# Kernel tuning notes

Hardware: AMD Instinct MI355X
Metric: run time of the kernel (lower is better)

The kernel has to match this reference:

```python
import jax, jax.numpy as jnp
import numpy as np

B, L, H = 2, 2048, 1024
NH, KVH = 16, 4
HD = H // NH          # 64
G = NH // KVH         # 4 query heads per kv head


def setup_inputs() -> dict:
    key = jax.random.key(0)
    ks = jax.random.split(key, 10)
    s = 0.02
    return {
        "hidden_states": jax.random.normal(ks[0], (B, L, H), dtype=jnp.float32),
        "attention_mask": jnp.zeros((B, 1, L, L), dtype=jnp.float32),
        "Wq": jax.random.normal(ks[1], (H, H), dtype=jnp.float32) * s,
        "bq": jnp.zeros((H,), dtype=jnp.float32),
        "Wk": jax.random.normal(ks[2], (KVH * HD, H), dtype=jnp.float32) * s,
        "bk": jnp.zeros((KVH * HD,), dtype=jnp.float32),
        "Wv": jax.random.normal(ks[3], (KVH * HD, H), dtype=jnp.float32) * s,
        "bv": jnp.zeros((KVH * HD,), dtype=jnp.float32),
        "Wo": jax.random.normal(ks[4], (H, H), dtype=jnp.float32) * s,
        "bo": jnp.zeros((H,), dtype=jnp.float32),
    }


def reference(hidden_states, attention_mask, Wq, bq, Wk, bk, Wv, bv, Wo, bo):
    x = hidden_states
    # projections (torch Linear: x @ W.T + b)
    q = (x @ Wq.T + bq).reshape(B, L, NH, HD).transpose(0, 2, 1, 3)   # [B,NH,L,HD]
    k = (x @ Wk.T + bk).reshape(B, L, KVH, HD).transpose(0, 2, 1, 3)  # [B,KVH,L,HD]
    v = (x @ Wv.T + bv).reshape(B, L, KVH, HD).transpose(0, 2, 1, 3)
    # GQA: group query heads per kv head instead of repeat_interleave (same math)
    qg = q.reshape(B, KVH, G, L, HD)
    scores = jnp.einsum("bkgqd,bkld->bkgql", qg, k) / jnp.sqrt(jnp.float32(HD))
    scores = scores + attention_mask[:, :, None, :, :]  # mask broadcasts over heads
    attn = jax.nn.softmax(scores, axis=-1)              # dropout p=0 -> identity
    ctx = jnp.einsum("bkgql,bkld->bkgqd", attn, v)      # [B,KVH,G,L,HD]
    ctx = ctx.reshape(B, NH, L, HD).transpose(0, 2, 1, 3).reshape(B, L, H)
    return ctx @ Wo.T + bo
```

## Files before the change

### kernel.cpp

```cpp
#include <hip/hip_runtime.h>

#define B_   2
#define L_   2048
#define H_   1024
#define NH_  16
#define KVH_ 4
#define HD_  64

typedef short short8 __attribute__((ext_vector_type(8)));
typedef float f32x4 __attribute__((ext_vector_type(4)));
typedef float f32x16 __attribute__((ext_vector_type(16)));
typedef unsigned short u16x4 __attribute__((ext_vector_type(4)));

#define LOG2E 1.4426950408889634f
#define QSC   0.18033688011112042f
#define MFMA   __builtin_amdgcn_mfma_f32_16x16x32_bf16
#define MFMA32 __builtin_amdgcn_mfma_f32_32x32x16_bf16

#if __has_builtin(__builtin_amdgcn_exp2f)
#define EXP2(x) __builtin_amdgcn_exp2f(x)
#else
#define EXP2(x) exp2f(x)
#endif

static __device__ __forceinline__ unsigned short f2bf(float f) {
  unsigned int u = __float_as_uint(f);
  u += 0x7FFFu + ((u >> 16) & 1u);
  return (unsigned short)(u >> 16);
}

static __device__ __forceinline__ unsigned int cvtpk(float lo, float hi) {
  unsigned int r;
  asm("v_cvt_pk_bf16_f32 %0, %1, %2" : "=v"(r) : "v"(lo), "v"(hi));
  return r;
}

static __device__ __forceinline__ void plswap(unsigned int& a, unsigned int& b) {
  asm("v_permlane32_swap_b32 %0, %1" : "+v"(a), "+v"(b));
}

static __device__ __forceinline__ short8 mk8(unsigned int w0, unsigned int w1,
                                             unsigned int w2, unsigned int w3) {
  union { unsigned int u[4]; short8 s; } x;
  x.u[0] = w0; x.u[1] = w1; x.u[2] = w2; x.u[3] = w3;
  return x.s;
}

static __device__ __forceinline__ void gload_lds16(const void* g, void* l) {
  __builtin_amdgcn_global_load_lds(
      (const __attribute__((address_space(1))) unsigned int*)g,
      (__attribute__((address_space(3))) unsigned int*)l, 16, 0, 0);
}

__global__ __launch_bounds__(256) void k_prep(const float* __restrict__ x,
                                              const float* __restrict__ Wq,
                                              const float* __restrict__ Wk,
                                              const float* __restrict__ Wv,
                                              const float* __restrict__ Wo,
                                              const float* __restrict__ mask,
                                              unsigned short* __restrict__ xb,
                                              unsigned short* __restrict__ wcat,
                                              unsigned short* __restrict__ wo_b,
                                              unsigned char* __restrict__ flags) {
  const int blk = blockIdx.x;
  const int t = threadIdx.x;
  if (blk < 4096) {
    size_t i = ((size_t)blk * 256 + t) * 4;
    float4 v = *(const float4*)(x + i);
    u16x4 o = { f2bf(v.x), f2bf(v.y), f2bf(v.z), f2bf(v.w) };
    *(u16x4*)(xb + i) = o;
  } else if (blk < 6656) {
    int r = blk - 4096;
    int c = t * 4;
    const float* src;
    unsigned short* dst;
    if (r < 1024)      { src = Wq + (size_t)r * 1024;          dst = wcat + (size_t)r * 1024; }
    else if (r < 1280) { src = Wk + (size_t)(r - 1024) * 1024; dst = wcat + (size_t)r * 1024; }
    else if (r < 1536) { src = Wv + (size_t)(r - 1280) * 1024; dst = wcat + (size_t)r * 1024; }
    else               { src = Wo + (size_t)(r - 1536) * 1024; dst = wo_b + (size_t)(r - 1536) * 1024; }
    float4 v = *(const float4*)(src + c);
    u16x4 o = { f2bf(v.x), f2bf(v.y), f2bf(v.z), f2bf(v.w) };
    *(u16x4*)(dst + c) = o;
  } else {
    const int mb = blk - 6656;
    const int b = mb >> 10, qb = (mb >> 5) & 31, kb = mb & 31;
    const float* base = mask + ((size_t)b * L_ + qb * 64) * L_ + kb * 64;
    const int r0 = t >> 4, c = (t & 15) * 4;
    bool nz = false;
#pragma unroll
    for (int i = 0; i < 4; ++i) {
      float4 v = *(const float4*)(base + (size_t)(r0 + i * 16) * L_ + c);
      nz |= (v.x != 0.f) | (v.y != 0.f) | (v.z != 0.f) | (v.w != 0.f);
    }
    __shared__ int anyv;
    if (t == 0) anyv = 0;
    __syncthreads();
    if (__any(nz) && (t & 63) == 0) atomicOr(&anyv, 1);
    __syncthreads();
    if (t == 0) flags[mb] = (unsigned char)anyv;
  }
}

template <int MODE>
__global__ __launch_bounds__(256) void k_gemm(const unsigned short* __restrict__ A,
                                              const unsigned short* __restrict__ Bt,
                                              const float* __restrict__ bias0,
                                              const float* __restrict__ bias1,
                                              const float* __restrict__ bias2,
                                              unsigned short* __restrict__ q_ws,
                                              unsigned short* __restrict__ k_ws,
                                              unsigned short* __restrict__ vt_ws,
                                              float* __restrict__ outp) {
  const int bn = blockIdx.x, bm = blockIdx.y;
  const int t = threadIdx.x;
  const int lane = t & 63, li = lane & 15, g = lane >> 4;
  const int wid = t >> 6, wr = wid >> 1, wc = wid & 1;
  __shared__ unsigned short lds_a[128 * 32];
  __shared__ unsigned short lds_b[128 * 32];

  const f32x4 z = {0.f, 0.f, 0.f, 0.f};
  f32x4 acc[4][4];
#pragma unroll
  for (int m = 0; m < 4; ++m)
#pragma unroll
    for (int n = 0; n < 4; ++n) acc[m][n] = z;

  const int c0 = t, c1 = 256 + t;
  const int r0 = c0 >> 2, o0 = (c0 & 3) * 8;
  const int r1 = c1 >> 2, o1 = (c1 & 3) * 8;
  const unsigned short* a0p = A + (size_t)(bm * 128 + r0) * 1024 + o0;
  const unsigned short* a1p = A + (size_t)(bm * 128 + r1) * 1024 + o1;
  const unsigned short* b0p = Bt + (size_t)(bn * 128 + r0) * 1024 + o0;
  const unsigned short* b1p = Bt + (size_t)(bn * 128 + r1) * 1024 + o1;

  for (int kt = 0; kt < 1024; kt += 32) {
    gload_lds16(a0p + kt, &lds_a[c0 * 8]);
    gload_lds16(a1p + kt, &lds_a[c1 * 8]);
    gload_lds16(b0p + kt, &lds_b[c0 * 8]);
    gload_lds16(b1p + kt, &lds_b[c1 * 8]);
    __syncthreads();
    short8 af[4], bf[4];
#pragma unroll
    for (int m = 0; m < 4; ++m) af[m] = *(const short8*)&lds_a[(wr * 64 + m * 16 + li) * 32 + g * 8];
#pragma unroll
    for (int n = 0; n < 4; ++n) bf[n] = *(const short8*)&lds_b[(wc * 64 + n * 16 + li) * 32 + g * 8];
#pragma unroll
    for (int m = 0; m < 4; ++m)
#pragma unroll
      for (int n = 0; n < 4; ++n)
        acc[m][n] = MFMA(af[m], bf[n], acc[m][n], 0, 0, 0);
    __syncthreads();
  }

#pragma unroll
  for (int m = 0; m < 4; ++m) {
    const int row0 = bm * 128 + wr * 64 + m * 16 + 4 * g;
#pragma unroll
    for (int n = 0; n < 4; ++n) {
      const int col = bn * 128 + wc * 64 + n * 16 + li;
      f32x4 v = acc[m][n];
      if (MODE == 1) {
        const float bias = bias0[col];
#pragma unroll
        for (int r = 0; r < 4; ++r) outp[(size_t)(row0 + r) * 1024 + col] = v[r] + bias;
      } else {
        if (col < 1024) {
          const float bias = bias0[col];
#pragma unroll
          for (int r = 0; r < 4; ++r) q_ws[(size_t)(row0 + r) * 1024 + col] = f2bf((v[r] + bias) * QSC);
        } else if (col < 1280) {
          const int cc = col - 1024;
          const float bias = bias1[cc];
#pragma unroll
          for (int r = 0; r < 4; ++r) k_ws[(size_t)(row0 + r) * 256 + cc] = f2bf(v[r] + bias);
        } else {
          const int cc = col - 1280;
          const float bias = bias2[cc];
          const int kvh = cc >> 6, d = cc & 63;
          const int b = row0 >> 11, l0 = row0 & 2047;
          u16x4 pk = { f2bf(v[0] + bias), f2bf(v[1] + bias), f2bf(v[2] + bias), f2bf(v[3] + bias) };
          *(u16x4*)(vt_ws + ((size_t)((b * KVH_ + kvh) * 64 + d)) * 2048 + l0) = pk;
        }
      }
    }
  }
}

__global__ __launch_bounds__(512, 4) void k_attn(const unsigned short* __restrict__ q_ws,
                                                 const unsigned short* __restrict__ k_ws,
                                                 const unsigned short* __restrict__ vt_ws,
                                                 const float* __restrict__ mask,
                                                 const unsigned char* __restrict__ mflags,
                                                 unsigned short* __restrict__ ctx) {
  const int bk = blockIdx.x;
  const int qt = blockIdx.y;
  const int b = bk >> 2, kvh = bk & 3;
  const int t = threadIdx.x;
  const int wid = t >> 6, lane = t & 63;
  const int l31 = lane & 31, g1 = lane >> 5;
  const int h = wid & 3, kh = wid >> 2;

  __shared__ unsigned short smem[16384];
  __shared__ float lred[4][64];

  const unsigned short* qbase = q_ws + ((size_t)b * L_ + qt * 32 + l31) * H_ +
                                (kvh * 4 + h) * 64 + g1 * 8;
  short8 qf[4];
#pragma unroll
  for (int ks = 0; ks < 4; ++ks) qf[ks] = *(const short8*)(qbase + ks * 16);

  const unsigned int* fp = (const unsigned int*)(mflags + b * 1024 + (qt >> 1) * 32);
  unsigned int fm = 0;
#pragma unroll
  for (int w = 0; w < 8; ++w) {
    unsigned int wv = fp[w];
    fm |= ((wv & 0x000000FFu) ? 1u : 0u) << (w * 4 + 0);
    fm |= ((wv & 0x0000FF00u) ? 1u : 0u) << (w * 4 + 1);
    fm |= ((wv & 0x00FF0000u) ? 1u : 0u) << (w * 4 + 2);
    fm |= ((wv & 0xFF000000u) ? 1u : 0u) << (w * 4 + 3);
  }
  fm = __builtin_amdgcn_readfirstlane(fm);

  const int srow = t >> 3, sgr = t & 7;
  const int swz = (sgr ^ (srow & 7)) * 8;
  const unsigned short* ksrc = k_ws + ((size_t)b * L_ + srow) * 256 + kvh * 64 + swz;
  const unsigned short* vsrc = vt_ws + ((size_t)(b * KVH_ + kvh) * 64 + srow) * 2048 + swz;

  const f32x16 z16 = {0,0,0,0,0,0,0,0,0,0,0,0,0,0,0,0};
  f32x16 o_[2];
  o_[0] = z16; o_[1] = z16;
  float l_part = 0.f;

  const int rK = kh * 32 + l31, swK = rK & 7;
  const int swV = l31 & 7;

#define STAGE(buf, kt)                                                        \
  {                                                                           \
    unsigned short* dk = smem + (buf) * 8192;                                 \
    gload_lds16(ksrc + (size_t)(kt) * 64 * 256, dk + t * 8);                  \
    gload_lds16(vsrc + (kt) * 64, dk + 4096 + t * 8);                         \
  }

  STAGE(0, 0);
  __syncthreads();

#pragma unroll 1
  for (int kt = 0; kt < 32; ++kt) {
    const int cur = kt & 1;
    if (kt + 1 < 32) STAGE(cur ^ 1, kt + 1);

    const unsigned short* lk = smem + cur * 8192;
    const unsigned short* lv = lk + 4096;

    short8 kf[4];
#pragma unroll
    for (int ks = 0; ks < 4; ++ks)
      kf[ks] = *(const short8*)&lk[rK * 64 + ((ks * 2 + g1) ^ swK) * 8];
    short8 vf[2][2];
#pragma unroll
    for (int db = 0; db < 2; ++db)
#pragma unroll
      for (int s = 0; s < 2; ++s)
        vf[db][s] = *(const short8*)&lv[(db * 32 + l31) * 64 + ((kh * 4 + s * 2 + g1) ^ swV) * 8];

    f32x16 sv = z16;
    __builtin_amdgcn_s_setprio(1);
#pragma unroll
    for (int ks = 0; ks < 4; ++ks) sv = MFMA32(kf[ks], qf[ks], sv, 0, 0, 0);
    __builtin_amdgcn_s_setprio(0);

    if (fm & (1u << kt)) {
      const float* mrow = mask + ((size_t)b * L_ + qt * 32 + l31) * L_ + kt * 64 + kh * 32 + g1 * 4;
#pragma unroll
      for (int rg = 0; rg < 4; ++rg) {
        float4 mv = *(const float4*)(mrow + rg * 8);
#pragma unroll
        for (int j = 0; j < 4; ++j) sv[rg * 4 + j] = fmaf((&mv.x)[j], LOG2E, sv[rg * 4 + j]);
      }
    }

    float e[16];
#pragma unroll
    for (int r = 0; r < 16; ++r) e[r] = EXP2(sv[r]);
    l_part += (((e[0] + e[1]) + (e[2] + e[3])) + ((e[4] + e[5]) + (e[6] + e[7]))) +
              (((e[8] + e[9]) + (e[10] + e[11])) + ((e[12] + e[13]) + (e[14] + e[15])));
    unsigned int w0 = cvtpk(e[0], e[1]),   w1 = cvtpk(e[2], e[3]);
    unsigned int w2 = cvtpk(e[4], e[5]),   w3 = cvtpk(e[6], e[7]);
    unsigned int w4 = cvtpk(e[8], e[9]),   w5 = cvtpk(e[10], e[11]);
    unsigned int w6 = cvtpk(e[12], e[13]), w7 = cvtpk(e[14], e[15]);
    plswap(w0, w2); plswap(w1, w3);
    plswap(w4, w6); plswap(w5, w7);
    short8 pa0 = mk8(w0, w1, w2, w3);
    short8 pa1 = mk8(w4, w5, w6, w7);

    __builtin_amdgcn_s_setprio(1);
#pragma unroll
    for (int db = 0; db < 2; ++db) {
      o_[db] = MFMA32(vf[db][0], pa0, o_[db], 0, 0, 0);
      o_[db] = MFMA32(vf[db][1], pa1, o_[db], 0, 0, 0);
    }
    __builtin_amdgcn_s_setprio(0);

    __syncthreads();
  }
#undef STAGE

  float lt = l_part + __shfl_xor(l_part, 32);
  float* red = (float*)smem;

  if (kh == 1) {
    lred[h][lane] = lt;
#pragma unroll
    for (int db = 0; db < 2; ++db)
#pragma unroll
      for (int w4 = 0; w4 < 4; ++w4) {
        f32x4 pv = { o_[db][w4 * 4 + 0], o_[db][w4 * 4 + 1],
                     o_[db][w4 * 4 + 2], o_[db][w4 * 4 + 3] };
        *(f32x4*)&red[(((h * 2 + db) * 4 + w4) * 64 + lane) * 4] = pv;
      }
  }
  __syncthreads();

  if (kh == 0) {
    const float inv = 1.f / (lt + lred[h][lane]);
#pragma unroll
    for (int db = 0; db < 2; ++db) {
      f32x16 acc = o_[db];
#pragma unroll
      for (int w4 = 0; w4 < 4; ++w4) {
        f32x4 pv = *(const f32x4*)&red[(((h * 2 + db) * 4 + w4) * 64 + lane) * 4];
#pragma unroll
        for (int j = 0; j < 4; ++j) acc[w4 * 4 + j] += pv[j];
      }
      unsigned short* cp = ctx + ((size_t)b * L_ + qt * 32 + l31) * H_ +
                           (kvh * 4 + h) * 64 + db * 32 + g1 * 4;
#pragma unroll
      for (int k4 = 0; k4 < 4; ++k4) {
        unsigned int a0 = cvtpk(acc[4 * k4 + 0] * inv, acc[4 * k4 + 1] * inv);
        unsigned int a1 = cvtpk(acc[4 * k4 + 2] * inv, acc[4 * k4 + 3] * inv);
        *(unsigned int*)(cp + 8 * k4) = a0;
        *(unsigned int*)(cp + 8 * k4 + 2) = a1;
      }
    }
  }
}

extern "C" void kernel_launch(void* const* d_in, const int* in_sizes, int n_in,
                              void* d_out, int out_size, void* d_ws, size_t ws_size,
                              hipStream_t stream) {
  const float* x    = (const float*)d_in[0];
  const float* mask = (const float*)d_in[1];
  const float* Wq   = (const float*)d_in[2];
  const float* bq   = (const float*)d_in[3];
  const float* Wk   = (const float*)d_in[4];
  const float* bk   = (const float*)d_in[5];
  const float* Wv   = (const float*)d_in[6];
  const float* bv   = (const float*)d_in[7];
  const float* Wo   = (const float*)d_in[8];
  const float* bo   = (const float*)d_in[9];
  float* out = (float*)d_out;

  char* ws = (char*)d_ws;
  unsigned short* xb    = (unsigned short*)(ws);
  unsigned short* ctx   = xb;
  unsigned short* wcat  = (unsigned short*)(ws + 8388608);
  unsigned short* wo_b  = (unsigned short*)(ws + 11534336);
  unsigned short* q_ws  = (unsigned short*)(ws + 13631488);
  unsigned short* k_ws  = (unsigned short*)(ws + 22020096);
  unsigned short* vt_ws = (unsigned short*)(ws + 24117248);
  unsigned char*  mflg  = (unsigned char*)(ws + 26214400);

  k_prep<<<dim3(8704), dim3(256), 0, stream>>>(x, Wq, Wk, Wv, Wo, mask, xb, wcat, wo_b, mflg);
  k_gemm<0><<<dim3(12, 32), dim3(256), 0, stream>>>(xb, wcat, bq, bk, bv, q_ws, k_ws, vt_ws, nullptr);
  k_attn<<<dim3(8, 64), dim3(512), 0, stream>>>(q_ws, k_ws, vt_ws, mask, mflg, ctx);
  k_gemm<1><<<dim3(8, 32), dim3(256), 0, stream>>>(ctx, wo_b, bo, nullptr, nullptr,
                                                   nullptr, nullptr, nullptr, out);
}
```

Baseline: 114.5 us.

## Widen GEMM K-tile with swizzled LDS and register-stage attention K/V prefetch

The projection GEMM now stages a 64-wide K slice per iteration with an XOR-swizzled LDS layout. This halves the number of barriers per output tile and is meant to cut LDS bank conflicts. The attention loop replaces direct global-to-LDS loads with register staging two tiles ahead, written to the alternate LDS buffer after fragment reads. The loop then uses a hand-placed waitcnt and s_barrier instead of __syncthreads. This deepens prefetch to hide global latency, at the cost of extra registers and relying on manual waitcnt correctness.

```diff
diff --git a/kernel.cpp b/kernel.cpp
--- a/kernel.cpp
+++ b/kernel.cpp
@@ -115,8 +115,8 @@
   const int t = threadIdx.x;
   const int lane = t & 63, li = lane & 15, g = lane >> 4;
   const int wid = t >> 6, wr = wid >> 1, wc = wid & 1;
-  __shared__ unsigned short lds_a[128 * 32];
-  __shared__ unsigned short lds_b[128 * 32];
+  __shared__ unsigned short lds_a[128 * 64];
+  __shared__ unsigned short lds_b[128 * 64];
 
   const f32x4 z = {0.f, 0.f, 0.f, 0.f};
   f32x4 acc[4][4];
@@ -125,30 +125,41 @@
 #pragma unroll
     for (int n = 0; n < 4; ++n) acc[m][n] = z;
 
-  const int c0 = t, c1 = 256 + t;
-  const int r0 = c0 >> 2, o0 = (c0 & 3) * 8;
-  const int r1 = c1 >> 2, o1 = (c1 & 3) * 8;
-  const unsigned short* a0p = A + (size_t)(bm * 128 + r0) * 1024 + o0;
-  const unsigned short* a1p = A + (size_t)(bm * 128 + r1) * 1024 + o1;
-  const unsigned short* b0p = Bt + (size_t)(bn * 128 + r0) * 1024 + o0;
-  const unsigned short* b1p = Bt + (size_t)(bn * 128 + r1) * 1024 + o1;
-
-  for (int kt = 0; kt < 1024; kt += 32) {
-    gload_lds16(a0p + kt, &lds_a[c0 * 8]);
-    gload_lds16(a1p + kt, &lds_a[c1 * 8]);
-    gload_lds16(b0p + kt, &lds_b[c0 * 8]);
-    gload_lds16(b1p + kt, &lds_b[c1 * 8]);
+  const unsigned short* asrc[4];
+  const unsigned short* bsrc[4];
+  int ldst[4];
+#pragma unroll
+  for (int c = 0; c < 4; ++c) {
+    const int idx = c * 256 + t, row = idx >> 3, sl = idx & 7;
+    const int gcol = (sl ^ (row & 7)) * 8;
+    asrc[c] = A  + (size_t)(bm * 128 + row) * 1024 + gcol;
+    bsrc[c] = Bt + (size_t)(bn * 128 + row) * 1024 + gcol;
+    ldst[c] = idx * 8;
+  }
+  const int rs = li & 7;
+
+  for (int kt = 0; kt < 1024; kt += 64) {
+#pragma unroll
+    for (int c = 0; c < 4; ++c) {
+      gload_lds16(asrc[c] + kt, &lds_a[ldst[c]]);
+      gload_lds16(bsrc[c] + kt, &lds_b[ldst[c]]);
+    }
     __syncthreads();
-    short8 af[4], bf[4];
-#pragma unroll
-    for (int m = 0; m < 4; ++m) af[m] = *(const short8*)&lds_a[(wr * 64 + m * 16 + li) * 32 + g * 8];
-#pragma unroll
-    for (int n = 0; n < 4; ++n) bf[n] = *(const short8*)&lds_b[(wc * 64 + n * 16 + li) * 32 + g * 8];
-#pragma unroll
-    for (int m = 0; m < 4; ++m)
+#pragma unroll
+    for (int ks = 0; ks < 2; ++ks) {
+      short8 af[4], bf[4];
+#pragma unroll
+      for (int m = 0; m < 4; ++m)
+        af[m] = *(const short8*)&lds_a[(wr * 64 + m * 16 + li) * 64 + (((ks * 4 + g) ^ rs) * 8)];
 #pragma unroll
       for (int n = 0; n < 4; ++n)
-        acc[m][n] = MFMA(af[m], bf[n], acc[m][n], 0, 0, 0);
+        bf[n] = *(const short8*)&lds_b[(wc * 64 + n * 16 + li) * 64 + (((ks * 4 + g) ^ rs) * 8)];
+#pragma unroll
+      for (int m = 0; m < 4; ++m)
+#pragma unroll
+        for (int n = 0; n < 4; ++n)
+          acc[m][n] = MFMA(af[m], bf[n], acc[m][n], 0, 0, 0);
+    }
     __syncthreads();
   }
 
@@ -234,21 +245,21 @@
   const int rK = kh * 32 + l31, swK = rK & 7;
   const int swV = l31 & 7;
 
-#define STAGE(buf, kt)                                                        \
-  {                                                                           \
-    unsigned short* dk = smem + (buf) * 8192;                                 \
-    gload_lds16(ksrc + (size_t)(kt) * 64 * 256, dk + t * 8);                  \
-    gload_lds16(vsrc + (kt) * 64, dk + 4096 + t * 8);                         \
-  }
-
-  STAGE(0, 0);
+  short8 kst, vst;
+#define LOADR(kt) { kst = *(const short8*)(ksrc + (size_t)(kt) * 16384); \
+                    vst = *(const short8*)(vsrc + (kt) * 64); }
+#define WRITES(buf) { unsigned short* dk = smem + (buf) * 8192;          \
+                      *(short8*)(dk + t * 8) = kst;                      \
+                      *(short8*)(dk + 4096 + t * 8) = vst; }
+
+  LOADR(0);
+  WRITES(0);
+  LOADR(1);
   __syncthreads();
 
 #pragma unroll 1
   for (int kt = 0; kt < 32; ++kt) {
     const int cur = kt & 1;
-    if (kt + 1 < 32) STAGE(cur ^ 1, kt + 1);
-
     const unsigned short* lk = smem + cur * 8192;
     const unsigned short* lv = lk + 4096;
 
@@ -262,6 +273,10 @@
 #pragma unroll
       for (int s = 0; s < 2; ++s)
         vf[db][s] = *(const short8*)&lv[(db * 32 + l31) * 64 + ((kh * 4 + s * 2 + g1) ^ swV) * 8];
+
+    asm volatile("s_waitcnt vmcnt(0)" ::: "memory");
+    if (kt + 1 < 32) WRITES(cur ^ 1);
+    if (kt + 2 < 32) LOADR(kt + 2);
 
     f32x16 sv = z16;
     __builtin_amdgcn_s_setprio(1);
@@ -301,9 +316,12 @@
     }
     __builtin_amdgcn_s_setprio(0);
 
-    __syncthreads();
-  }
-#undef STAGE
+    asm volatile("s_waitcnt lgkmcnt(0)" ::: "memory");
+    __builtin_amdgcn_s_barrier();
+    __builtin_amdgcn_sched_barrier(0);
+  }
+#undef LOADR
+#undef WRITES
 
   float lt = l_part + __shfl_xor(l_part, 32);
   float* red = (float*)smem;
```

New measurement: 106.5 us. -7.0%, faster.
